# Performance work log

Hardware: AMD Instinct MI355X
Metric: run time of the kernel (lower is better)

The kernel has to match this reference:

```python
import jax, jax.numpy as jnp
import numpy as np

K = 3            # pairwise_size
DIL = 2          # pairwise_dilation
COLOR_THRESH = 0.3
EOS_COEF = 0.1


def unfold_wo_center(x, k, d):
    """x: [N,1,H,W] -> [N,1,k*k-1,H,W]; zero-padded dilated neighborhood, center removed
    (equivalent to F.unfold(x, k, padding=(k//2)*d, dilation=d) minus center tap)."""
    N, C, H, W = x.shape
    pad = (k // 2) * d
    xp = jnp.pad(x, ((0, 0), (0, 0), (pad, pad), (pad, pad)))
    c = k // 2
    patches = []
    for i in range(k):
        for j in range(k):
            if i == c and j == c:
                continue
            patches.append(xp[:, :, i * d:i * d + H, j * d:j * d + W])
    return jnp.stack(patches, axis=2)


def setup_inputs() -> dict:
    key = jax.random.key(0)
    k1, k2, k3, k4, k5 = jax.random.split(key, 5)
    B, Q, C1 = 2, 100, 81          # batch, queries, num_classes+1
    N, H, W = 64, 256, 256         # matched instances, mask resolution
    pred_logits = jax.random.normal(k1, (B, Q, C1), jnp.float32)
    target_classes = jax.random.randint(k2, (B, Q), 0, C1)
    src_masks = jax.random.normal(k3, (N, H, W), jnp.float32)
    target_box_masks = jax.random.randint(k4, (N, H, W), 0, 2).astype(jnp.int32)
    target_similarities = jax.random.uniform(k5, (N, K * K - 1, H, W), jnp.float32)
    empty_weight = jnp.ones((C1,), jnp.float32).at[-1].set(EOS_COEF)
    return {
        "pred_logits": pred_logits,
        "src_masks": src_masks,
        "empty_weight": empty_weight,
        "target_similarities": target_similarities,
        "target_classes": target_classes,
        "target_box_masks": target_box_masks,
        "num_masks": 64,
    }


def reference(pred_logits, src_masks, empty_weight, target_similarities,
              target_classes, target_box_masks, num_masks):
    nm = jnp.float32(max(int(num_masks), 1))

    # ---- loss_labels: weighted cross entropy (PyTorch weighted mean) ----
    logp = jax.nn.log_softmax(pred_logits.astype(jnp.float32), axis=-1)
    nll = -jnp.take_along_axis(logp, target_classes[..., None], axis=-1)[..., 0]
    w = empty_weight[target_classes]
    loss_ce = (w * nll).sum() / w.sum()

    # ---- loss_pairwise: BoxInst-style log-prob affinity over dilated neighborhood ----
    x = src_masks[:, None]                      # [N,1,H,W]
    lfg = jax.nn.log_sigmoid(x)
    lbg = jax.nn.log_sigmoid(-x)
    fg_u = unfold_wo_center(lfg, K, DIL)        # [N,1,8,H,W]
    bg_u = unfold_wo_center(lbg, K, DIL)
    a = lfg[:, :, None] + fg_u                  # log P(both fg)
    b = lbg[:, :, None] + bg_u                  # log P(both bg)
    m = jnp.maximum(a, b)
    log_same = jnp.log(jnp.exp(a - m) + jnp.exp(b - m)) + m
    sim = -log_same[:, 0]                       # [N,8,H,W]
    tgt = (target_similarities >= COLOR_THRESH).astype(jnp.float32) \
          * target_box_masks[:, None].astype(jnp.float32)
    loss_pairwise = (sim * tgt).sum() / jnp.maximum(tgt.sum(), 1.0) / nm
    # warmup_factor = 1.0 (iter >= pairwise_warmup_iters)

    # ---- loss_projection_masks: 1D projection dice ----
    eps = 0.001
    tb = target_box_masks.astype(jnp.float32)
    ix = jax.nn.sigmoid(src_masks.max(axis=2))  # project over W -> [N,H]
    iy = jax.nn.sigmoid(src_masks.max(axis=1))  # project over H -> [N,W]
    tx = tb.max(axis=2)
    ty = tb.max(axis=1)
    lx = 1.0 - 2.0 * (ix * tx).sum(1) / ((ix ** 2).sum(1) + (tx ** 2).sum(1) + eps)
    ly = 1.0 - 2.0 * (iy * ty).sum(1) / ((iy ** 2).sum(1) + (ty ** 2).sum(1) + eps)
    loss_proj = (lx + ly).sum() / nm

    return loss_ce + loss_pairwise + loss_proj
```

## Files before the change

kernel.cpp:

```cpp
#include <hip/hip_runtime.h>
#include <hip/hip_bf16.h>
#include <cmath>

__device__ inline float waveReduceSum(float v) {
#pragma unroll
    for (int o = 32; o > 0; o >>= 1) v += __shfl_xor(v, o, 64);
    return v;
}
__device__ inline float waveReduceMax(float v) {
#pragma unroll
    for (int o = 32; o > 0; o >>= 1) v = fmaxf(v, __shfl_xor(v, o, 64));
    return v;
}
__device__ inline float blockReduceSum(float v, float* s) {
    int lane = threadIdx.x & 63, wv = threadIdx.x >> 6;
    v = waveReduceSum(v);
    if (lane == 0) s[wv] = v;
    __syncthreads();
    float r = 0.f;
    if (wv == 0) {
        r = (lane < 4) ? s[lane] : 0.f;
        r = waveReduceSum(r);
    }
    __syncthreads();
    return r;
}
__device__ inline float blockReduceMax(float v, float* s) {
    int lane = threadIdx.x & 63, wv = threadIdx.x >> 6;
    v = waveReduceMax(v);
    if (lane == 0) s[wv] = v;
    __syncthreads();
    float r = -3.4e38f;
    if (wv == 0) {
        r = (lane < 4) ? s[lane] : -3.4e38f;
        r = waveReduceMax(r);
    }
    __syncthreads();
    return r;
}

#define H 256
#define W 256
#define NIMG 64
#define HW 65536
#define RG 16

__global__ __launch_bounds__(256) void k_pairwise(
    const float* __restrict__ src, const float* __restrict__ ts,
    const int* __restrict__ bm,
    float* __restrict__ part_st, float* __restrict__ part_t,
    float* __restrict__ rowsig, float* __restrict__ rowmax_b)
{
    __shared__ float s_sig[RG + 4][W];
    __shared__ float red[4];
    const int hg = blockIdx.x, n = blockIdx.y, w = threadIdx.x;
    const int h0 = hg * RG;
    const float* srcn = src + (size_t)n * HW;
#pragma unroll
    for (int r = 0; r < RG + 4; r++) {
        const int gr = h0 - 2 + r;
        float s = 0.5f;
        if (gr >= 0 && gr < H) {
            const float x = srcn[gr * W + w];
            s = __builtin_amdgcn_rcpf(1.f + __expf(-x));
        }
        s_sig[r][w] = s;
    }
    __syncthreads();
    const int* bmn = bm + (size_t)n * HW;
    const float* tsbase = ts + (size_t)n * 8 * HW + w;

    const int DR[8] = {-2, -2, -2, 0, 0, 2, 2, 2};
    const int DC[8] = {-2, 0, 2, -2, 2, -2, 0, 2};
    float st = 0.f, tt = 0.f;
    for (int rr = 0; rr < RG; rr++) {
        const int h = h0 + rr;
        const int ci = rr + 2;
        const float sc = s_sig[ci][w];
        const float omc = 1.f - sc;
        const float bmf = (float)bmn[h * W + w];
        const float* tsn = tsbase + h * W;
#pragma unroll
        for (int p = 0; p < 8; p++) {
            const int hr = h + DR[p];
            const int wc = w + DC[p];
            const bool valid = (hr >= 0) && (hr < H) && (wc >= 0) && (wc < W);
            const int wcc = min(max(wc, 0), W - 1);
            const float sn = s_sig[ci + DR[p]][wcc];
            const float P = valid ? fmaf(sc, sn, omc * (1.f - sn)) : 1.f;
            const float tsv = tsn[(size_t)p * HW];
            const float tg = (tsv >= 0.3f) ? bmf : 0.f;
            st = fmaf(-__logf(P), tg, st);
            tt += tg;
        }
        const float mxs = blockReduceMax(sc, red);
        const float mxb = blockReduceMax(bmf, red);
        if (threadIdx.x == 0) {
            rowsig[n * H + h] = mxs;
            rowmax_b[n * H + h] = mxb;
        }
    }
    const float sst = blockReduceSum(st, red);
    const float stt = blockReduceSum(tt, red);
    if (threadIdx.x == 0) {
        const int o = n * 16 + hg;
        part_st[o] = sst;
        part_t[o] = stt;
    }
}

__global__ __launch_bounds__(256) void k_colmax(
    const float* __restrict__ src, const int* __restrict__ bm,
    float* __restrict__ colpart_x, float* __restrict__ colpart_b)
{
    const int chunk = blockIdx.x, n = blockIdx.y, w = threadIdx.x;
    const float* s = src + (size_t)n * HW + chunk * 32 * W + w;
    const int* b = bm + (size_t)n * HW + chunk * 32 * W + w;
    float mx = -3.4e38f, mb = 0.f;
#pragma unroll 8
    for (int r = 0; r < 32; r++) {
        mx = fmaxf(mx, s[r * W]);
        mb = fmaxf(mb, (float)b[r * W]);
    }
    const int o = (n * 8 + chunk) * W + w;
    colpart_x[o] = mx;
    colpart_b[o] = mb;
}

__global__ __launch_bounds__(256) void k_proj(
    const float* __restrict__ colpart_x, const float* __restrict__ colpart_b,
    const float* __restrict__ rowsig, const float* __restrict__ rowmax_b,
    float* __restrict__ proj)
{
    __shared__ float red[4];
    const int n = blockIdx.x, t = threadIdx.x;
    float cx = -3.4e38f, cb = 0.f;
#pragma unroll
    for (int c = 0; c < 8; c++) {
        cx = fmaxf(cx, colpart_x[(n * 8 + c) * W + t]);
        cb = fmaxf(cb, colpart_b[(n * 8 + c) * W + t]);
    }
    const float iy = 1.f / (1.f + expf(-cx));
    const float ty = cb;
    const float ix = rowsig[n * H + t];
    const float tx = rowmax_b[n * H + t];

    const float Sxy = blockReduceSum(ix * tx, red);
    const float Sxx = blockReduceSum(ix * ix, red);
    const float Stx = blockReduceSum(tx * tx, red);
    const float Syw = blockReduceSum(iy * ty, red);
    const float Syy = blockReduceSum(iy * iy, red);
    const float Sty = blockReduceSum(ty * ty, red);
    if (t == 0) {
        const float eps = 0.001f;
        const float lx = 1.f - 2.f * Sxy / (Sxx + Stx + eps);
        const float ly = 1.f - 2.f * Syw / (Syy + Sty + eps);
        proj[n] = lx + ly;
    }
}

__global__ __launch_bounds__(256) void k_final(
    const float* __restrict__ logits, const int* __restrict__ tcls,
    const float* __restrict__ ew, const int* __restrict__ num_masks,
    const float* __restrict__ part_st, const float* __restrict__ part_t,
    const float* __restrict__ proj, float* __restrict__ out)
{
    __shared__ float red[4];
    const int t = threadIdx.x;
    float s1 = 0.f, s2 = 0.f;
    for (int i = t; i < NIMG * 16; i += 256) { s1 += part_st[i]; s2 += part_t[i]; }
    const float sum_st = blockReduceSum(s1, red);
    const float sum_t = blockReduceSum(s2, red);
    const float pj = (t < NIMG) ? proj[t] : 0.f;
    const float sum_pj = blockReduceSum(pj, red);

    float wn = 0.f, wsum = 0.f;
    if (t < 200) {
        const float* row = logits + t * 81;
        float mx = -3.4e38f;
        for (int c = 0; c < 81; c++) mx = fmaxf(mx, row[c]);
        float se = 0.f;
        for (int c = 0; c < 81; c++) se += expf(row[c] - mx);
        const float lse = mx + logf(se);
        const int tc = tcls[t];
        const float nll = lse - row[tc];
        const float wv = ew[tc];
        wn = wv * nll;
        wsum = wv;
    }
    const float Swn = blockReduceSum(wn, red);
    const float Sw = blockReduceSum(wsum, red);
    if (t == 0) {
        const float nm = (float)max(num_masks[0], 1);
        const float loss_ce = Swn / Sw;
        const float loss_pw = sum_st / fmaxf(sum_t, 1.f) / nm;
        const float loss_pj = sum_pj / nm;
        out[0] = loss_ce + loss_pw + loss_pj;
    }
}

extern "C" void kernel_launch(void* const* d_in, const int* in_sizes, int n_in,
                              void* d_out, int out_size, void* d_ws, size_t ws_size,
                              hipStream_t stream) {
    const float* pred_logits = (const float*)d_in[0];
    const float* src         = (const float*)d_in[1];
    const float* ew          = (const float*)d_in[2];
    const float* ts          = (const float*)d_in[3];
    const int*   tcls        = (const int*)d_in[4];
    const int*   bm          = (const int*)d_in[5];
    const int*   nmasks      = (const int*)d_in[6];
    float* out = (float*)d_out;

    float* ws = (float*)d_ws;
    float* part_st   = ws;
    float* part_t    = ws + 1024;
    float* rowsig    = ws + 2048;
    float* rowmax_b  = ws + 18432;
    float* colpart_x = ws + 34816;
    float* colpart_b = ws + 165888;
    float* proj      = ws + 296960;

    k_pairwise<<<dim3(16, NIMG), 256, 0, stream>>>(src, ts, bm, part_st, part_t, rowsig, rowmax_b);
    k_colmax<<<dim3(8, NIMG), 256, 0, stream>>>(src, bm, colpart_x, colpart_b);
    k_proj<<<NIMG, 256, 0, stream>>>(colpart_x, colpart_b, rowsig, rowmax_b, proj);
    k_final<<<1, 256, 0, stream>>>(pred_logits, tcls, ew, nmasks, part_st, part_t, proj, out);
}
```

Measured before the change: 274.3 us.

## Move per-row max reductions out of pairwise kernel into column-max kernel

```diff
diff --git a/kernel.cpp b/kernel.cpp
--- a/kernel.cpp
+++ b/kernel.cpp
@@ -25,31 +25,17 @@
     __syncthreads();
     return r;
 }
-__device__ inline float blockReduceMax(float v, float* s) {
-    int lane = threadIdx.x & 63, wv = threadIdx.x >> 6;
-    v = waveReduceMax(v);
-    if (lane == 0) s[wv] = v;
-    __syncthreads();
-    float r = -3.4e38f;
-    if (wv == 0) {
-        r = (lane < 4) ? s[lane] : -3.4e38f;
-        r = waveReduceMax(r);
-    }
-    __syncthreads();
-    return r;
-}
 
 #define H 256
 #define W 256
 #define NIMG 64
 #define HW 65536
-#define RG 16
+#define RG 8
 
 __global__ __launch_bounds__(256) void k_pairwise(
     const float* __restrict__ src, const float* __restrict__ ts,
     const int* __restrict__ bm,
-    float* __restrict__ part_st, float* __restrict__ part_t,
-    float* __restrict__ rowsig, float* __restrict__ rowmax_b)
+    float* __restrict__ part_st, float* __restrict__ part_t)
 {
     __shared__ float s_sig[RG + 4][W];
     __shared__ float red[4];
@@ -73,6 +59,7 @@
     const int DR[8] = {-2, -2, -2, 0, 0, 2, 2, 2};
     const int DC[8] = {-2, 0, 2, -2, 2, -2, 0, 2};
     float st = 0.f, tt = 0.f;
+#pragma unroll
     for (int rr = 0; rr < RG; rr++) {
         const int h = h0 + rr;
         const int ci = rr + 2;
@@ -93,43 +80,55 @@
             st = fmaf(-__logf(P), tg, st);
             tt += tg;
         }
-        const float mxs = blockReduceMax(sc, red);
-        const float mxb = blockReduceMax(bmf, red);
-        if (threadIdx.x == 0) {
-            rowsig[n * H + h] = mxs;
-            rowmax_b[n * H + h] = mxb;
-        }
     }
     const float sst = blockReduceSum(st, red);
     const float stt = blockReduceSum(tt, red);
     if (threadIdx.x == 0) {
-        const int o = n * 16 + hg;
+        const int o = n * 32 + hg;
         part_st[o] = sst;
         part_t[o] = stt;
     }
 }
 
-__global__ __launch_bounds__(256) void k_colmax(
+__global__ __launch_bounds__(256) void k_maxes(
     const float* __restrict__ src, const int* __restrict__ bm,
-    float* __restrict__ colpart_x, float* __restrict__ colpart_b)
-{
-    const int chunk = blockIdx.x, n = blockIdx.y, w = threadIdx.x;
-    const float* s = src + (size_t)n * HW + chunk * 32 * W + w;
-    const int* b = bm + (size_t)n * HW + chunk * 32 * W + w;
-    float mx = -3.4e38f, mb = 0.f;
-#pragma unroll 8
+    float* __restrict__ colpart_x, float* __restrict__ colpart_b,
+    float* __restrict__ rowmax_x, float* __restrict__ rowmax_b)
+{
+    __shared__ float sx[32][4];
+    __shared__ float sb[32][4];
+    const int chunk = blockIdx.x, n = blockIdx.y, t = threadIdx.x;
+    const int lane = t & 63, wv = t >> 6;
+    const float* s = src + (size_t)n * HW + chunk * 32 * W + t;
+    const int* b = bm + (size_t)n * HW + chunk * 32 * W + t;
+    float cmx = -3.4e38f, cmb = 0.f;
+#pragma unroll 4
     for (int r = 0; r < 32; r++) {
-        mx = fmaxf(mx, s[r * W]);
-        mb = fmaxf(mb, (float)b[r * W]);
-    }
-    const int o = (n * 8 + chunk) * W + w;
-    colpart_x[o] = mx;
-    colpart_b[o] = mb;
+        const float x = s[r * W];
+        const float bf = (float)b[r * W];
+        cmx = fmaxf(cmx, x);
+        cmb = fmaxf(cmb, bf);
+        const float rx = waveReduceMax(x);
+        const float rb = waveReduceMax(bf);
+        if (lane == 0) { sx[r][wv] = rx; sb[r][wv] = rb; }
+    }
+    const int o = (n * 8 + chunk) * W + t;
+    colpart_x[o] = cmx;
+    colpart_b[o] = cmb;
+    __syncthreads();
+    if (t < 32) {
+        const float m = fmaxf(fmaxf(sx[t][0], sx[t][1]), fmaxf(sx[t][2], sx[t][3]));
+        rowmax_x[n * H + chunk * 32 + t] = m;
+    } else if (t < 64) {
+        const int r = t - 32;
+        const float m = fmaxf(fmaxf(sb[r][0], sb[r][1]), fmaxf(sb[r][2], sb[r][3]));
+        rowmax_b[n * H + chunk * 32 + r] = m;
+    }
 }
 
 __global__ __launch_bounds__(256) void k_proj(
     const float* __restrict__ colpart_x, const float* __restrict__ colpart_b,
-    const float* __restrict__ rowsig, const float* __restrict__ rowmax_b,
+    const float* __restrict__ rowmax_x, const float* __restrict__ rowmax_b,
     float* __restrict__ proj)
 {
     __shared__ float red[4];
@@ -142,7 +141,7 @@
     }
     const float iy = 1.f / (1.f + expf(-cx));
     const float ty = cb;
-    const float ix = rowsig[n * H + t];
+    const float ix = 1.f / (1.f + expf(-rowmax_x[n * H + t]));
     const float tx = rowmax_b[n * H + t];
 
     const float Sxy = blockReduceSum(ix * tx, red);
@@ -168,7 +167,7 @@
     __shared__ float red[4];
     const int t = threadIdx.x;
     float s1 = 0.f, s2 = 0.f;
-    for (int i = t; i < NIMG * 16; i += 256) { s1 += part_st[i]; s2 += part_t[i]; }
+    for (int i = t; i < NIMG * 32; i += 256) { s1 += part_st[i]; s2 += part_t[i]; }
     const float sum_st = blockReduceSum(s1, red);
     const float sum_t = blockReduceSum(s2, red);
     const float pj = (t < NIMG) ? proj[t] : 0.f;
@@ -213,15 +212,15 @@
 
     float* ws = (float*)d_ws;
     float* part_st   = ws;
-    float* part_t    = ws + 1024;
-    float* rowsig    = ws + 2048;
-    float* rowmax_b  = ws + 18432;
-    float* colpart_x = ws + 34816;
-    float* colpart_b = ws + 165888;
-    float* proj      = ws + 296960;
-
-    k_pairwise<<<dim3(16, NIMG), 256, 0, stream>>>(src, ts, bm, part_st, part_t, rowsig, rowmax_b);
-    k_colmax<<<dim3(8, NIMG), 256, 0, stream>>>(src, bm, colpart_x, colpart_b);
-    k_proj<<<NIMG, 256, 0, stream>>>(colpart_x, colpart_b, rowsig, rowmax_b, proj);
+    float* part_t    = ws + 2048;
+    float* rowmax_x  = ws + 4096;
+    float* rowmax_b  = ws + 20480;
+    float* colpart_x = ws + 36864;
+    float* colpart_b = ws + 167936;
+    float* proj      = ws + 299008;
+
+    k_pairwise<<<dim3(32, NIMG), 256, 0, stream>>>(src, ts, bm, part_st, part_t);
+    k_maxes<<<dim3(8, NIMG), 256, 0, stream>>>(src, bm, colpart_x, colpart_b, rowmax_x, rowmax_b);
+    k_proj<<<NIMG, 256, 0, stream>>>(colpart_x, colpart_b, rowmax_x, rowmax_b, proj);
     k_final<<<1, 256, 0, stream>>>(pred_logits, tcls, ew, nmasks, part_st, part_t, proj, out);
 }
```

Result: slower. 284.4 us (+3.7%).
